# Optimization experiments

Measured on AMD Instinct MI355X. Metric: run time of the kernel, lower is better.

The kernel has to match this reference:

```python
import jax, jax.numpy as jnp
import numpy as np
import math


def _rotary_cos_sin(seq_len, head_dim, base=10000.0):
    # Matches SEDD's Rotary: cos/sin of shape [1, s, 3, 1, d], with the
    # v-slice (index 2 of the 'three' axis) set to identity (cos=1, sin=0).
    inv_freq = 1.0 / (base ** (np.arange(0, head_dim, 2, dtype=np.float32) / head_dim))
    t = np.arange(seq_len, dtype=np.float32)
    freqs = np.einsum('i,j->ij', t, inv_freq)          # [s, d/2]
    emb = np.concatenate([freqs, freqs], axis=-1)       # [s, d]
    cos = np.tile(np.cos(emb)[None, :, None, None, :], (1, 1, 3, 1, 1))
    sin = np.tile(np.sin(emb)[None, :, None, None, :], (1, 1, 3, 1, 1))
    cos[:, :, 2] = 1.0
    sin[:, :, 2] = 0.0
    return jnp.asarray(cos, dtype=jnp.float32), jnp.asarray(sin, dtype=jnp.float32)


def _rotate_half(x):
    x1, x2 = jnp.split(x, 2, axis=-1)
    return jnp.concatenate([-x2, x1], axis=-1)


def setup_inputs() -> dict:
    key = jax.random.key(0)
    B, S, H, D = 2, 2048, 12, 64
    k1, k2 = jax.random.split(key)
    qkv = jax.random.normal(k1, (B, S, 3, H, D), dtype=jnp.float32)
    cos, sin = _rotary_cos_sin(S, D)
    seqlens = jax.random.randint(k2, (B,), 1024, S + 1).astype(jnp.int32)
    return {"qkv": qkv, "cos": cos, "sin": sin, "seqlens": seqlens}


def reference(qkv, cos, sin, seqlens):
    B, S, _, H, D = qkv.shape
    # rotary applied to all of qkv; v slice of cos/sin is identity
    qkv = qkv * cos + _rotate_half(qkv) * sin
    # split and reshape to (b, h, s, d)
    q = jnp.transpose(qkv[:, :, 0], (0, 2, 1, 3))
    k = jnp.transpose(qkv[:, :, 1], (0, 2, 1, 3))
    v = jnp.transpose(qkv[:, :, 2], (0, 2, 1, 3))
    # padding mask from ragged seqlens
    valid = jnp.arange(S, dtype=jnp.int32)[None, :] < seqlens[:, None]   # [b, s]
    mask = valid[:, :, None] & valid[:, None, :]                          # [b, i, j]
    attn_logits = jnp.einsum('bhid,bhjd->bhij', q, k) / math.sqrt(D)
    attn_logits = jnp.where(mask[:, None, :, :], attn_logits, -1e10)
    attn = jax.nn.softmax(attn_logits, axis=-1)
    x = jnp.einsum('bhij,bhjd->bhid', attn, v)
    return x, attn_logits
```

## Files before the change

kernel.cpp:

```cpp
#include <hip/hip_runtime.h>
#include <hip/hip_bf16.h>
#include <math.h>

#define SLEN 2048
#define NH   12
#define NB   2
#define DH   64
#define IT   64
#define JT   64
#define LDK  72
#define NWAVE 4

typedef __bf16 bfx8 __attribute__((ext_vector_type(8)));
typedef float  f32x4 __attribute__((ext_vector_type(4)));

__device__ __forceinline__ void stage_rot(const float* __restrict__ qkv,
                                          const float* __restrict__ cosb,
                                          const float* __restrict__ sinb,
                                          int b, int h, int s_base, int t,
                                          __bf16* dst, int tid)
{
    const int r  = tid >> 2;
    const int d0 = (tid & 3) * 16;
    const int s  = s_base + r;
    const float* src = qkv + (((size_t)((size_t)b * SLEN + s) * 3 + t) * NH + h) * DH;
    const float* cs  = cosb + ((size_t)s * 3 + t) * DH;
    const float* sn  = sinb + ((size_t)s * 3 + t) * DH;
#pragma unroll
    for (int dd = 0; dd < 16; dd += 4) {
        const int d = d0 + dd;
        float4 f  = *(const float4*)(src + d);
        float4 g  = *(const float4*)(src + (d ^ 32));
        float4 c4 = *(const float4*)(cs + d);
        float4 s4 = *(const float4*)(sn + d);
        const float sg = (d < 32) ? -1.f : 1.f;
        union { __bf16 hv[4]; uint2 u; } pk;
        pk.hv[0] = (__bf16)(f.x * c4.x + sg * g.x * s4.x);
        pk.hv[1] = (__bf16)(f.y * c4.y + sg * g.y * s4.y);
        pk.hv[2] = (__bf16)(f.z * c4.z + sg * g.z * s4.z);
        pk.hv[3] = (__bf16)(f.w * c4.w + sg * g.w * s4.w);
        *(uint2*)(dst + r * LDK + d) = pk.u;
    }
}

__global__ __launch_bounds__(256)
void ddit_attn(const float* __restrict__ qkv,
               const float* __restrict__ cosb,
               const float* __restrict__ sinb,
               const int*   __restrict__ seqlens,
               float* __restrict__ out_x,
               float* __restrict__ out_logits)
{
    __shared__ __align__(16) __bf16 Klds[IT * LDK];
    __shared__ __align__(16) __bf16 Vt[DH * LDK];
    __shared__ __align__(16) __bf16 Pbuf[NWAVE * 16 * LDK];

    const int tid  = threadIdx.x;
    const int wave = tid >> 6;
    const int lane = tid & 63;
    const int qd   = lane >> 4;
    const int m    = lane & 15;

    const int nIt = SLEN / IT;
    const int it  = blockIdx.x % nIt;
    const int bh  = blockIdx.x / nIt;
    const int h   = bh % NH;
    const int b   = bh / NH;
    const int i0  = it * IT;
    const int len = seqlens[b];

    float* logits_base = out_logits + (size_t)bh * SLEN * SLEN;

    stage_rot(qkv, cosb, sinb, b, h, i0, 0, Klds, tid);
    __syncthreads();
    bfx8 qfrag[2];
#pragma unroll
    for (int c = 0; c < 2; ++c)
        qfrag[c] = *(const bfx8*)&Klds[(wave * 16 + m) * LDK + c * 32 + qd * 8];

    float mrun[4], lrun[4];
    f32x4 acc[4];
#pragma unroll
    for (int r = 0; r < 4; ++r) { mrun[r] = -3.0e38f; lrun[r] = 0.f; }
#pragma unroll
    for (int c = 0; c < 4; ++c) acc[c] = (f32x4){0.f, 0.f, 0.f, 0.f};

    const int irow_base = i0 + wave * 16 + qd * 4;
    __bf16* myP = Pbuf + wave * 16 * LDK;

    for (int j0 = 0; j0 < SLEN; j0 += JT) {
        __syncthreads();
        stage_rot(qkv, cosb, sinb, b, h, j0, 1, Klds, tid);
        {
            const int r  = tid >> 2;
            const int d0 = (tid & 3) * 16;
            const int s  = j0 + r;
            const float* src = qkv + (((size_t)((size_t)b * SLEN + s) * 3 + 2) * NH + h) * DH;
#pragma unroll
            for (int dd = 0; dd < 16; dd += 4) {
                float4 f = *(const float4*)(src + d0 + dd);
                Vt[(d0 + dd + 0) * LDK + r] = (__bf16)f.x;
                Vt[(d0 + dd + 1) * LDK + r] = (__bf16)f.y;
                Vt[(d0 + dd + 2) * LDK + r] = (__bf16)f.z;
                Vt[(d0 + dd + 3) * LDK + r] = (__bf16)f.w;
            }
        }
        __syncthreads();

        f32x4 sacc[4];
#pragma unroll
        for (int t4 = 0; t4 < 4; ++t4) {
            sacc[t4] = (f32x4){0.f, 0.f, 0.f, 0.f};
#pragma unroll
            for (int c = 0; c < 2; ++c) {
                bfx8 kf = *(const bfx8*)&Klds[(t4 * 16 + m) * LDK + c * 32 + qd * 8];
                sacc[t4] = __builtin_amdgcn_mfma_f32_16x16x32_bf16(qfrag[c], kf, sacc[t4], 0, 0, 0);
            }
        }

        float ls[4][4];
#pragma unroll
        for (int t4 = 0; t4 < 4; ++t4) {
            const int jG = j0 + t4 * 16 + m;
            const bool vj = jG < len;
#pragma unroll
            for (int r = 0; r < 4; ++r) {
                const int iG = irow_base + r;
                const bool ok = vj && (iG < len);
                const float lv = ok ? sacc[t4][r] * 0.125f : -1.0e10f;
                ls[t4][r] = lv;
                logits_base[(size_t)iG * SLEN + jG] = lv;
            }
        }

#pragma unroll
        for (int r = 0; r < 4; ++r) {
            float mt = fmaxf(fmaxf(ls[0][r], ls[1][r]), fmaxf(ls[2][r], ls[3][r]));
#pragma unroll
            for (int off = 1; off < 16; off <<= 1)
                mt = fmaxf(mt, __shfl_xor(mt, off));
            const float mn = fmaxf(mrun[r], mt);
            const float al = __expf(mrun[r] - mn);
            float p[4], ps = 0.f;
#pragma unroll
            for (int t4 = 0; t4 < 4; ++t4) { p[t4] = __expf(ls[t4][r] - mn); ps += p[t4]; }
#pragma unroll
            for (int off = 1; off < 16; off <<= 1)
                ps += __shfl_xor(ps, off);
            lrun[r] = lrun[r] * al + ps;
            mrun[r] = mn;
#pragma unroll
            for (int c = 0; c < 4; ++c) acc[c][r] *= al;
#pragma unroll
            for (int t4 = 0; t4 < 4; ++t4)
                myP[(qd * 4 + r) * LDK + t4 * 16 + m] = (__bf16)p[t4];
        }

#pragma unroll
        for (int kc = 0; kc < 2; ++kc) {
            bfx8 pf = *(const bfx8*)&myP[m * LDK + kc * 32 + qd * 8];
#pragma unroll
            for (int c = 0; c < 4; ++c) {
                bfx8 vf = *(const bfx8*)&Vt[(c * 16 + m) * LDK + kc * 32 + qd * 8];
                acc[c] = __builtin_amdgcn_mfma_f32_16x16x32_bf16(pf, vf, acc[c], 0, 0, 0);
            }
        }
    }

#pragma unroll
    for (int r = 0; r < 4; ++r) {
        const int iG = irow_base + r;
        const float inv = 1.f / lrun[r];
#pragma unroll
        for (int c = 0; c < 4; ++c)
            out_x[((size_t)bh * SLEN + iG) * DH + c * 16 + m] = acc[c][r] * inv;
    }
}

extern "C" void kernel_launch(void* const* d_in, const int* in_sizes, int n_in,
                              void* d_out, int out_size, void* d_ws, size_t ws_size,
                              hipStream_t stream) {
    const float* qkv     = (const float*)d_in[0];
    const float* cosb    = (const float*)d_in[1];
    const float* sinb    = (const float*)d_in[2];
    const int*   seqlens = (const int*)d_in[3];
    float* out_x      = (float*)d_out;
    float* out_logits = out_x + (size_t)NB * NH * SLEN * DH;

    dim3 grid(NB * NH * (SLEN / IT));
    dim3 block(256);
    ddit_attn<<<grid, block, 0, stream>>>(qkv, cosb, sinb, seqlens, out_x, out_logits);
}
```

Measured before the change: 637.2 us.

## Precompute rotary Q/K and transposed V in bf16 with a prep kernel

Adds a prep kernel that applies rotary embedding once and writes bf16 Q, K and a transposed V into workspace. The attention kernel then loads K and V fragments directly from global memory into registers, with no LDS staging and no block barriers in the inner loop. Block IDs are also remapped across eight groups, likely to spread heads over XCDs for better L2 locality. This removes the repeated fp32 reads and rotary work on K/V that each of the 32 query tiles per head used to redo. In exchange it adds a second launch and a workspace round trip, and relies on global and L2 latency for the fragment loads.

Measured after the change: 583.6 us. 1.09x faster.

```diff
diff --git a/kernel.cpp b/kernel.cpp
--- a/kernel.cpp
+++ b/kernel.cpp
@@ -8,52 +8,88 @@
 #define DH   64
 #define IT   64
 #define JT   64
-#define LDK  72
 #define NWAVE 4
+#define LDP  72
 
 typedef __bf16 bfx8 __attribute__((ext_vector_type(8)));
 typedef float  f32x4 __attribute__((ext_vector_type(4)));
 
-__device__ __forceinline__ void stage_rot(const float* __restrict__ qkv,
-                                          const float* __restrict__ cosb,
-                                          const float* __restrict__ sinb,
-                                          int b, int h, int s_base, int t,
-                                          __bf16* dst, int tid)
-{
-    const int r  = tid >> 2;
-    const int d0 = (tid & 3) * 16;
-    const int s  = s_base + r;
-    const float* src = qkv + (((size_t)((size_t)b * SLEN + s) * 3 + t) * NH + h) * DH;
-    const float* cs  = cosb + ((size_t)s * 3 + t) * DH;
-    const float* sn  = sinb + ((size_t)s * 3 + t) * DH;
-#pragma unroll
-    for (int dd = 0; dd < 16; dd += 4) {
-        const int d = d0 + dd;
-        float4 f  = *(const float4*)(src + d);
-        float4 g  = *(const float4*)(src + (d ^ 32));
-        float4 c4 = *(const float4*)(cs + d);
-        float4 s4 = *(const float4*)(sn + d);
-        const float sg = (d < 32) ? -1.f : 1.f;
-        union { __bf16 hv[4]; uint2 u; } pk;
-        pk.hv[0] = (__bf16)(f.x * c4.x + sg * g.x * s4.x);
-        pk.hv[1] = (__bf16)(f.y * c4.y + sg * g.y * s4.y);
-        pk.hv[2] = (__bf16)(f.z * c4.z + sg * g.z * s4.z);
-        pk.hv[3] = (__bf16)(f.w * c4.w + sg * g.w * s4.w);
-        *(uint2*)(dst + r * LDK + d) = pk.u;
-    }
-}
-
 __global__ __launch_bounds__(256)
-void ddit_attn(const float* __restrict__ qkv,
+void ddit_prep(const float* __restrict__ qkv,
                const float* __restrict__ cosb,
                const float* __restrict__ sinb,
+               __bf16* __restrict__ Qr, __bf16* __restrict__ Kr,
+               __bf16* __restrict__ Vt)
+{
+    __shared__ __align__(16) __bf16 Vlds[64 * LDP];
+    const int tid = threadIdx.x;
+    const int nS  = SLEN / 64;
+    const int s0  = (blockIdx.x % nS) * 64;
+    const int bh  = blockIdx.x / nS;
+    const int h   = bh % NH;
+    const int b   = bh / NH;
+    const int r   = tid >> 2;
+    const int d0  = (tid & 3) * 16;
+    const int s   = s0 + r;
+
+#pragma unroll
+    for (int t = 0; t < 2; ++t) {
+        const float* src = qkv + (((size_t)((size_t)b * SLEN + s) * 3 + t) * NH + h) * DH;
+        const float* cs  = cosb + ((size_t)s * 3 + t) * DH;
+        const float* sn  = sinb + ((size_t)s * 3 + t) * DH;
+        union { __bf16 hv[16]; uint4 u4[2]; } pk;
+#pragma unroll
+        for (int dd = 0; dd < 16; dd += 4) {
+            const int d = d0 + dd;
+            float4 f  = *(const float4*)(src + d);
+            float4 g  = *(const float4*)(src + (d ^ 32));
+            float4 c4 = *(const float4*)(cs + d);
+            float4 s4 = *(const float4*)(sn + d);
+            const float sg = (d < 32) ? -1.f : 1.f;
+            pk.hv[dd + 0] = (__bf16)(f.x * c4.x + sg * g.x * s4.x);
+            pk.hv[dd + 1] = (__bf16)(f.y * c4.y + sg * g.y * s4.y);
+            pk.hv[dd + 2] = (__bf16)(f.z * c4.z + sg * g.z * s4.z);
+            pk.hv[dd + 3] = (__bf16)(f.w * c4.w + sg * g.w * s4.w);
+        }
+        __bf16* dst = (t == 0 ? Qr : Kr) + ((size_t)bh * SLEN + s) * DH + d0;
+        *(uint4*)(dst + 0) = pk.u4[0];
+        *(uint4*)(dst + 8) = pk.u4[1];
+    }
+
+    {
+        const float* src = qkv + (((size_t)((size_t)b * SLEN + s) * 3 + 2) * NH + h) * DH;
+#pragma unroll
+        for (int dd = 0; dd < 16; dd += 4) {
+            float4 f = *(const float4*)(src + d0 + dd);
+            union { __bf16 hv[4]; uint2 u; } pk;
+            pk.hv[0] = (__bf16)f.x; pk.hv[1] = (__bf16)f.y;
+            pk.hv[2] = (__bf16)f.z; pk.hv[3] = (__bf16)f.w;
+            *(uint2*)(Vlds + r * LDP + d0 + dd) = pk.u;
+        }
+    }
+    __syncthreads();
+    {
+        const int dv   = tid >> 2;
+        const int soff = (tid & 3) * 16;
+        union { __bf16 hv[16]; uint4 u4[2]; } pk;
+#pragma unroll
+        for (int j = 0; j < 16; ++j)
+            pk.hv[j] = Vlds[(soff + j) * LDP + dv];
+        __bf16* dst = Vt + ((size_t)bh * DH + dv) * SLEN + s0 + soff;
+        *(uint4*)(dst + 0) = pk.u4[0];
+        *(uint4*)(dst + 8) = pk.u4[1];
+    }
+}
+
+__global__ __launch_bounds__(256)
+void ddit_attn(const __bf16* __restrict__ Qr,
+               const __bf16* __restrict__ Kr,
+               const __bf16* __restrict__ Vt,
                const int*   __restrict__ seqlens,
                float* __restrict__ out_x,
                float* __restrict__ out_logits)
 {
-    __shared__ __align__(16) __bf16 Klds[IT * LDK];
-    __shared__ __align__(16) __bf16 Vt[DH * LDK];
-    __shared__ __align__(16) __bf16 Pbuf[NWAVE * 16 * LDK];
+    __shared__ __align__(16) __bf16 Pbuf[NWAVE * 16 * LDP];
 
     const int tid  = threadIdx.x;
     const int wave = tid >> 6;
@@ -61,22 +97,25 @@
     const int qd   = lane >> 4;
     const int m    = lane & 15;
 
-    const int nIt = SLEN / IT;
-    const int it  = blockIdx.x % nIt;
-    const int bh  = blockIdx.x / nIt;
-    const int h   = bh % NH;
-    const int b   = bh / NH;
-    const int i0  = it * IT;
-    const int len = seqlens[b];
-
+    const int nIt   = SLEN / IT;
+    const int gridN = NB * NH * nIt;
+    const int bid   = blockIdx.x;
+    const int nid   = (bid & 7) * (gridN >> 3) + (bid >> 3);
+    const int it    = nid % nIt;
+    const int bh    = nid / nIt;
+    const int b     = bh / NH;
+    const int i0    = it * IT;
+    const int len   = seqlens[b];
+
+    const __bf16* Qb = Qr + (size_t)bh * SLEN * DH;
+    const __bf16* Kb = Kr + (size_t)bh * SLEN * DH;
+    const __bf16* Vb = Vt + (size_t)bh * DH * SLEN;
     float* logits_base = out_logits + (size_t)bh * SLEN * SLEN;
 
-    stage_rot(qkv, cosb, sinb, b, h, i0, 0, Klds, tid);
-    __syncthreads();
     bfx8 qfrag[2];
 #pragma unroll
     for (int c = 0; c < 2; ++c)
-        qfrag[c] = *(const bfx8*)&Klds[(wave * 16 + m) * LDK + c * 32 + qd * 8];
+        qfrag[c] = *(const bfx8*)(Qb + (size_t)(i0 + wave * 16 + m) * DH + c * 32 + qd * 8);
 
     float mrun[4], lrun[4];
     f32x4 acc[4];
@@ -86,37 +125,31 @@
     for (int c = 0; c < 4; ++c) acc[c] = (f32x4){0.f, 0.f, 0.f, 0.f};
 
     const int irow_base = i0 + wave * 16 + qd * 4;
-    __bf16* myP = Pbuf + wave * 16 * LDK;
+    __bf16* myP = Pbuf + wave * 16 * LDP;
 
     for (int j0 = 0; j0 < SLEN; j0 += JT) {
-        __syncthreads();
-        stage_rot(qkv, cosb, sinb, b, h, j0, 1, Klds, tid);
-        {
-            const int r  = tid >> 2;
-            const int d0 = (tid & 3) * 16;
-            const int s  = j0 + r;
-            const float* src = qkv + (((size_t)((size_t)b * SLEN + s) * 3 + 2) * NH + h) * DH;
-#pragma unroll
-            for (int dd = 0; dd < 16; dd += 4) {
-                float4 f = *(const float4*)(src + d0 + dd);
-                Vt[(d0 + dd + 0) * LDK + r] = (__bf16)f.x;
-                Vt[(d0 + dd + 1) * LDK + r] = (__bf16)f.y;
-                Vt[(d0 + dd + 2) * LDK + r] = (__bf16)f.z;
-                Vt[(d0 + dd + 3) * LDK + r] = (__bf16)f.w;
-            }
-        }
-        __syncthreads();
+        bfx8 kf[4][2];
+#pragma unroll
+        for (int t4 = 0; t4 < 4; ++t4)
+#pragma unroll
+            for (int c = 0; c < 2; ++c)
+                kf[t4][c] = *(const bfx8*)(Kb + (size_t)(j0 + t4 * 16 + m) * DH + c * 32 + qd * 8);
 
         f32x4 sacc[4];
 #pragma unroll
         for (int t4 = 0; t4 < 4; ++t4) {
             sacc[t4] = (f32x4){0.f, 0.f, 0.f, 0.f};
 #pragma unroll
-            for (int c = 0; c < 2; ++c) {
-                bfx8 kf = *(const bfx8*)&Klds[(t4 * 16 + m) * LDK + c * 32 + qd * 8];
-                sacc[t4] = __builtin_amdgcn_mfma_f32_16x16x32_bf16(qfrag[c], kf, sacc[t4], 0, 0, 0);
-            }
-        }
+            for (int c = 0; c < 2; ++c)
+                sacc[t4] = __builtin_amdgcn_mfma_f32_16x16x32_bf16(qfrag[c], kf[t4][c], sacc[t4], 0, 0, 0);
+        }
+
+        bfx8 vf[2][4];
+#pragma unroll
+        for (int kc = 0; kc < 2; ++kc)
+#pragma unroll
+            for (int c = 0; c < 4; ++c)
+                vf[kc][c] = *(const bfx8*)(Vb + (size_t)(c * 16 + m) * SLEN + j0 + kc * 32 + qd * 8);
 
         float ls[4][4];
 #pragma unroll
@@ -153,17 +186,15 @@
             for (int c = 0; c < 4; ++c) acc[c][r] *= al;
 #pragma unroll
             for (int t4 = 0; t4 < 4; ++t4)
-                myP[(qd * 4 + r) * LDK + t4 * 16 + m] = (__bf16)p[t4];
+                myP[(qd * 4 + r) * LDP + t4 * 16 + m] = (__bf16)p[t4];
         }
 
 #pragma unroll
         for (int kc = 0; kc < 2; ++kc) {
-            bfx8 pf = *(const bfx8*)&myP[m * LDK + kc * 32 + qd * 8];
-#pragma unroll
-            for (int c = 0; c < 4; ++c) {
-                bfx8 vf = *(const bfx8*)&Vt[(c * 16 + m) * LDK + kc * 32 + qd * 8];
-                acc[c] = __builtin_amdgcn_mfma_f32_16x16x32_bf16(pf, vf, acc[c], 0, 0, 0);
-            }
+            bfx8 pf = *(const bfx8*)&myP[m * LDP + kc * 32 + qd * 8];
+#pragma unroll
+            for (int c = 0; c < 4; ++c)
+                acc[c] = __builtin_amdgcn_mfma_f32_16x16x32_bf16(pf, vf[kc][c], acc[c], 0, 0, 0);
         }
     }
 
@@ -187,7 +218,12 @@
     float* out_x      = (float*)d_out;
     float* out_logits = out_x + (size_t)NB * NH * SLEN * DH;
 
-    dim3 grid(NB * NH * (SLEN / IT));
+    const size_t perT = (size_t)NB * NH * SLEN * DH;
+    __bf16* Qr = (__bf16*)d_ws;
+    __bf16* Kr = Qr + perT;
+    __bf16* Vt = Kr + perT;
+
     dim3 block(256);
-    ddit_attn<<<grid, block, 0, stream>>>(qkv, cosb, sinb, seqlens, out_x, out_logits);
+    ddit_prep<<<dim3(NB * NH * (SLEN / 64)), block, 0, stream>>>(qkv, cosb, sinb, Qr, Kr, Vt);
+    ddit_attn<<<dim3(NB * NH * (SLEN / IT)), block, 0, stream>>>(Qr, Kr, Vt, seqlens, out_x, out_logits);
 }
```
